# Optimization experiments

Measured on AMD Instinct MI355X. Metric: run time of the kernel, lower is better.

Reference implementation:

```python
import jax, jax.numpy as jnp
import numpy as np


def setup_inputs() -> dict:
    key = jax.random.key(0)
    ks = jax.random.split(key, 7)
    B, T, C, D = 8, 2048, 1024, 128
    x = jax.random.normal(ks[0], (B, T, C), dtype=jnp.float32)
    # torch nn.Linear weights are [out_features, in_features]
    s = 1.0 / np.sqrt(C)
    Wq = jax.random.normal(ks[1], (D, C), dtype=jnp.float32) * s
    bq = jax.random.normal(ks[2], (D,), dtype=jnp.float32) * s
    Wk = jax.random.normal(ks[3], (D, C), dtype=jnp.float32) * s
    bk = jax.random.normal(ks[4], (D,), dtype=jnp.float32) * s
    Wv = jax.random.normal(ks[5], (D, C), dtype=jnp.float32) * s
    bv = jax.random.normal(ks[6], (D,), dtype=jnp.float32) * s
    return {"x": x, "Wq": Wq, "bq": bq, "Wk": Wk, "bk": bk, "Wv": Wv, "bv": bv}


def reference(x, Wq, bq, Wk, bk, Wv, bv):
    B, T, C = x.shape
    q = jnp.einsum('btc,dc->btd', x, Wq) + bq  # [B,T,D]
    k = jnp.einsum('btc,dc->btd', x, Wk) + bk
    v = jnp.einsum('btc,dc->btd', x, Wv) + bv
    scores = jnp.einsum('btd,bsd->bts', q, k)  # [B,T,T]
    causal = jnp.tril(jnp.ones((T, T), dtype=bool))
    masked = jnp.where(causal, scores, -jnp.inf)
    # NOTE: original scales by sqrt(key.weight.shape[-1]) == sqrt(emb_dim), AFTER masking
    scale = jnp.asarray(C, dtype=x.dtype) ** 0.5
    attn = jax.nn.softmax(masked / scale, axis=-1)
    return jnp.einsum('bts,bsd->btd', attn, v)
```

## Files before the change

### kernel.cpp

```cpp
#include <hip/hip_runtime.h>
#include <hip/hip_bf16.h>
#include <math.h>

typedef __bf16 bf16_t;
typedef __bf16 bf16x4 __attribute__((ext_vector_type(4)));
typedef __bf16 bf16x8 __attribute__((ext_vector_type(8)));
typedef float  f32x4  __attribute__((ext_vector_type(4)));
typedef float  f32x16 __attribute__((ext_vector_type(16)));
typedef int    v2i    __attribute__((ext_vector_type(2)));

static constexpr int Bz = 8, Tt = 2048, Cc = 1024, Dd = 128;
static constexpr int Mm = Bz * Tt;
static constexpr int NT128 = Tt / 128;

__device__ __forceinline__ bf16x8 lds_read8(const char* base, int byte) {
    return *(const bf16x8*)(base + byte);
}

__device__ __forceinline__ bf16x8 cvt8(float4 a, float4 b) {
    bf16x8 r;
    r[0] = (bf16_t)a.x; r[1] = (bf16_t)a.y; r[2] = (bf16_t)a.z; r[3] = (bf16_t)a.w;
    r[4] = (bf16_t)b.x; r[5] = (bf16_t)b.y; r[6] = (bf16_t)b.z; r[7] = (bf16_t)b.w;
    return r;
}

__device__ __forceinline__ unsigned cvtpk(float lo, float hi) {
    unsigned r;
    asm("v_cvt_pk_bf16_f32 %0, %1, %2" : "=v"(r) : "v"(lo), "v"(hi));
    return r;
}

typedef const __attribute__((address_space(1))) unsigned int* as1_u32p;
typedef __attribute__((address_space(3))) unsigned int* as3_u32p;

__device__ __forceinline__ void gload_lds16(const bf16_t* g, bf16_t* l) {
    __builtin_amdgcn_global_load_lds((as1_u32p)(const void*)g, (as3_u32p)(void*)l, 16, 0, 0);
}

__global__ __launch_bounds__(256) void wcvt_kernel(
    const float* __restrict__ Wq, const float* __restrict__ Wk,
    const float* __restrict__ Wv, bf16_t* __restrict__ Wp)
{
    int g = (blockIdx.x * 256 + threadIdx.x) * 4;
    int n = g >> 10;
    int k = g & 1023;
    int sel = n >> 7;
    const float* W = (sel == 0) ? Wq : (sel == 1) ? Wk : Wv;
    float4 f = *(const float4*)(W + (size_t)(n & 127) * 1024 + k);
    bf16x4 o; o[0] = (bf16_t)f.x; o[1] = (bf16_t)f.y; o[2] = (bf16_t)f.z; o[3] = (bf16_t)f.w;
    int ktile = k >> 6, kk = (k >> 5) & 1, hi = (k >> 3) & 3, e = k & 7;
    int ng = n >> 4, cg = ng / 12, ngl = ng % 12, lo = n & 15;
    size_t addr = (size_t)(((((ktile * 2 + cg) * 12 + ngl) * 2 + kk) * 4 + hi) * 16 + lo) * 8 + e;
    *(bf16x4*)(Wp + addr) = o;
}

__global__ __launch_bounds__(512, 4) void qkv_fused(
    const float* __restrict__ x, const bf16_t* __restrict__ Wp,
    const float* __restrict__ bq, const float* __restrict__ bk, const float* __restrict__ bv,
    bf16_t* __restrict__ qo, bf16_t* __restrict__ ko, bf16_t* __restrict__ vTo)
{
    const int m0  = blockIdx.x * 64;
    const int cg  = blockIdx.y;
    const int tid = threadIdx.x;
    const int lane = tid & 63;
    const int wv  = tid >> 6;
    const int wr  = wv >> 2;
    const int cw  = wv & 3;
    const int lo  = lane & 15;
    const int hi  = lane >> 4;

    __shared__ bf16_t Wl[2][12 * 2 * 512];
    __shared__ bf16_t Xs[2][64 * 64];

    f32x4 zero4 = {0.f, 0.f, 0.f, 0.f};
    f32x4 acc[2][3];
    #pragma unroll
    for (int i = 0; i < 2; i++)
        #pragma unroll
        for (int j = 0; j < 3; j++) acc[i][j] = zero4;

    const int xrow = tid >> 3;
    const int xcol = (tid & 7) * 8;

    float4 fx[2];
    auto load_x = [&](int t) {
        const float4* s = (const float4*)(x + (size_t)(m0 + xrow) * Cc + t * 64 + xcol);
        fx[0] = s[0]; fx[1] = s[1];
    };
    auto write_x = [&](int buf) {
        int byte = (xrow * 128 + xcol * 2) ^ ((xrow & 7) << 4);
        *(bf16x8*)((char*)Xs[buf] + byte) = cvt8(fx[0], fx[1]);
    };
    auto stage_W = [&](int buf, int t) {
        const bf16_t* base = Wp + (size_t)(t * 2 + cg) * 12288;
        #pragma unroll
        for (int i = 0; i < 3; i++) {
            int c = i * 8 + wv;
            gload_lds16(base + c * 512 + lane * 8, Wl[buf] + c * 512);
        }
    };
    auto compute = [&](int buf) {
        #pragma unroll
        for (int kk = 0; kk < 2; kk++) {
            int r0 = wr * 32 + lo;
            int r1 = wr * 32 + 16 + lo;
            bf16x8 af0 = lds_read8((char*)Xs[buf], (r0 * 128 + kk * 64 + hi * 16) ^ ((r0 & 7) << 4));
            bf16x8 af1 = lds_read8((char*)Xs[buf], (r1 * 128 + kk * 64 + hi * 16) ^ ((r1 & 7) << 4));
            #pragma unroll
            for (int j = 0; j < 3; j++) {
                bf16x8 bf = *(const bf16x8*)(Wl[buf] + ((cw * 3 + j) * 2 + kk) * 512 + lane * 8);
                acc[0][j] = __builtin_amdgcn_mfma_f32_16x16x32_bf16(af0, bf, acc[0][j], 0, 0, 0);
                acc[1][j] = __builtin_amdgcn_mfma_f32_16x16x32_bf16(af1, bf, acc[1][j], 0, 0, 0);
            }
        }
    };

    load_x(0);
    stage_W(0, 0);
    write_x(0);
    asm volatile("s_waitcnt lgkmcnt(0)" ::: "memory");
    __builtin_amdgcn_s_barrier();

    #pragma unroll 1
    for (int t = 0; t < 16; t++) {
        const int buf = t & 1;
        if (t < 15) {
            load_x(t + 1);
            stage_W(buf ^ 1, t + 1);
            asm volatile("s_waitcnt vmcnt(5)" ::: "memory");
        } else {
            asm volatile("s_waitcnt vmcnt(0)" ::: "memory");
        }
        __builtin_amdgcn_sched_barrier(0);
        compute(buf);
        if (t < 15) {
            write_x(buf ^ 1);
            asm volatile("s_waitcnt lgkmcnt(0)" ::: "memory");
            __builtin_amdgcn_s_barrier();
        }
    }

    #pragma unroll
    for (int j = 0; j < 3; j++) {
        int n = cg * 192 + cw * 48 + j * 16 + lo;
        int tsel = n >> 7, d = n & 127;
        const float* bp = (tsel == 0) ? bq : (tsel == 1) ? bk : bv;
        float bb = bp[d];
        #pragma unroll
        for (int i = 0; i < 2; i++)
            #pragma unroll
            for (int r = 0; r < 4; r++) {
                int m = m0 + wr * 32 + i * 16 + hi * 4 + r;
                float v = acc[i][j][r] + bb;
                if (tsel == 0)      qo[(size_t)m * Dd + d] = (bf16_t)v;
                else if (tsel == 1) ko[(size_t)m * Dd + d] = (bf16_t)v;
                else                vTo[(size_t)d * Mm + m] = (bf16_t)v;
            }
    }
}

__global__ __launch_bounds__(256, 2) void attn_kernel(
    const bf16_t* __restrict__ qi, const bf16_t* __restrict__ ki,
    const bf16_t* __restrict__ vTi,
    float* __restrict__ Opart, float* __restrict__ Mpart, float* __restrict__ Lpart,
    int nsplit)
{
    const int g   = blockIdx.x;
    const int per = nsplit * 8;
    const int qt  = (NT128 - 1) - g / per;
    const int rem = g % per;
    const int s   = rem >> 3;
    const int b   = rem & 7;
    const int nt  = 2 * qt + 2;
    const int t_lo = (s * nt) / nsplit;
    const int t_hi = ((s + 1) * nt) / nsplit;

    const int q0   = qt * 128;
    const int tid  = threadIdx.x;
    const int lane = tid & 63;
    const int w    = tid >> 6;
    const int rq   = lane & 31;
    const int dh   = lane >> 5;

    float* Ob = Opart + ((size_t)s * Mm + (size_t)b * Tt + q0) * Dd;
    float* Mb = Mpart + (size_t)s * Mm + (size_t)b * Tt + q0;
    float* Lb = Lpart + (size_t)s * Mm + (size_t)b * Tt + q0;

    if (t_lo >= t_hi) {
        float4 z = {0.f, 0.f, 0.f, 0.f};
        #pragma unroll
        for (int i = 0; i < 16; i++)
            ((float4*)Ob)[i * 256 + tid] = z;
        if (tid < 128) { Mb[tid] = -INFINITY; Lb[tid] = 0.f; }
        return;
    }

    __shared__ __align__(16) char smem[65536];

    const float SCALE = 1.4426950408889634f / 32.0f;
    const int qg = q0 + w * 32 + rq;
    const int qwmax = q0 + w * 32 + 31;

    bf16x8 qf[8];
    {
        const bf16_t* qrow = qi + (size_t)(b * Tt + qg) * Dd;
        #pragma unroll
        for (int ks = 0; ks < 8; ks++)
            qf[ks] = *(const bf16x8*)(qrow + ks * 16 + dh * 8);
    }

    f32x16 accO[4];
    #pragma unroll
    for (int ds = 0; ds < 4; ds++)
        #pragma unroll
        for (int e = 0; e < 16; e++) accO[ds][e] = 0.f;
    float mrun = -INFINITY, lrun = 0.f;

    const int krow = tid >> 2;
    const int kcol = (tid & 3) * 32;
    const int vrow = tid >> 1;
    const int vcol = (tid & 1) * 32;

    bf16x8 kr[4], vr[4];
    auto load_kv = [&](int t) {
        const int kv0 = t * 64;
        const bf16_t* ksrc = ki + (size_t)(b * Tt + kv0 + krow) * Dd + kcol;
        #pragma unroll
        for (int i = 0; i < 4; i++) kr[i] = *(const bf16x8*)(ksrc + i * 8);
        const bf16_t* vsrc = vTi + (size_t)vrow * Mm + (b * Tt + kv0 + vcol);
        #pragma unroll
        for (int i = 0; i < 4; i++) vr[i] = *(const bf16x8*)(vsrc + i * 8);
    };
    auto write_kv = [&](int buf) {
        char* Ksb = smem + buf * 16384;
        char* Vsb = smem + 32768 + buf * 16384;
        #pragma unroll
        for (int i = 0; i < 4; i++) {
            int byte = (krow * 256 + (kcol + i * 8) * 2) ^ ((krow & 15) << 4);
            *(bf16x8*)(Ksb + byte) = kr[i];
        }
        const int vlr = vrow & 63;
        const int vlc = (vrow >> 6) * 64 + vcol;
        #pragma unroll
        for (int i = 0; i < 4; i++) {
            int byte = (vlr * 256 + (vlc + i * 8) * 2) ^ ((vlr & 15) << 4);
            *(bf16x8*)(Vsb + byte) = vr[i];
        }
    };

    load_kv(t_lo);
    write_kv(0);
    int buf = 0;

    for (int t = t_lo; t < t_hi; t++) {
        const int kv0 = t * 64;
        const bool more = (t + 1 < t_hi);
        __syncthreads();
        if (more) load_kv(t + 1);

        if (kv0 <= qwmax) {
            const char* Ksb = smem + buf * 16384;
            const char* Vsb = smem + 32768 + buf * 16384;

            f32x16 accS0, accS1;
            #pragma unroll
            for (int e = 0; e < 16; e++) { accS0[e] = 0.f; accS1[e] = 0.f; }
            #pragma unroll
            for (int ks = 0; ks < 8; ks++) {
                int colb = (ks * 16 + dh * 8) * 2;
                bf16x8 kf0 = lds_read8(Ksb, ((rq)      * 256 + colb) ^ ((rq & 15) << 4));
                bf16x8 kf1 = lds_read8(Ksb, ((32 + rq) * 256 + colb) ^ ((rq & 15) << 4));
                accS0 = __builtin_amdgcn_mfma_f32_32x32x16_bf16(kf0, qf[ks], accS0, 0, 0, 0);
                accS1 = __builtin_amdgcn_mfma_f32_32x32x16_bf16(kf1, qf[ks], accS1, 0, 0, 0);
            }

            float pl[32];
            #pragma unroll
            for (int e = 0; e < 16; e++) {
                pl[e]      = accS0[e] * SCALE;
                pl[16 + e] = accS1[e] * SCALE;
            }
            if (kv0 + 63 > qg) {
                #pragma unroll
                for (int e = 0; e < 16; e++) {
                    int kg = kv0 + 8 * (e >> 2) + (e & 3) + 4 * dh;
                    if (kg > qg)      pl[e]      = -INFINITY;
                    if (kg + 32 > qg) pl[16 + e] = -INFINITY;
                }
            }

            float mt = pl[0];
            #pragma unroll
            for (int e = 1; e < 32; e++) mt = fmaxf(mt, pl[e]);
            mt = fmaxf(mt, __shfl_xor(mt, 32, 64));
            float mnew = fmaxf(mrun, mt);
            float muse = (mnew == -INFINITY) ? 0.f : mnew;
            float alpha = exp2f(mrun - muse);
            mrun = mnew;
            float ps = 0.f;
            #pragma unroll
            for (int e = 0; e < 32; e++) {
                float pv = exp2f(pl[e] - muse);
                pl[e] = pv;
                ps += pv;
            }
            lrun = alpha * lrun + ps;
            #pragma unroll
            for (int ds = 0; ds < 4; ds++)
                #pragma unroll
                for (int e = 0; e < 16; e++) accO[ds][e] *= alpha;

            unsigned u0[8], u1[8];
            #pragma unroll
            for (int gg = 0; gg < 8; gg++) {
                u0[gg] = cvtpk(pl[4 * gg + 0], pl[4 * gg + 1]);
                u1[gg] = cvtpk(pl[4 * gg + 2], pl[4 * gg + 3]);
            }
            bf16x8 pa[4];
            #pragma unroll
            for (int ks = 0; ks < 4; ks++) {
                v2i rA = __builtin_amdgcn_permlane32_swap((int)u0[2 * ks], (int)u0[2 * ks + 1], false, false);
                v2i rB = __builtin_amdgcn_permlane32_swap((int)u1[2 * ks], (int)u1[2 * ks + 1], false, false);
                union { unsigned wd[4]; bf16x8 v; } pu;
                pu.wd[0] = (unsigned)rA[0];
                pu.wd[1] = (unsigned)rB[0];
                pu.wd[2] = (unsigned)rA[1];
                pu.wd[3] = (unsigned)rB[1];
                pa[ks] = pu.v;
            }

            #pragma unroll
            for (int ds = 0; ds < 4; ds++) {
                int row  = (ds & 1) * 32 + rq;
                int cb   = (ds >> 1) * 64;
                #pragma unroll
                for (int ks = 0; ks < 4; ks++) {
                    int colb = (cb + ks * 16 + dh * 8) * 2;
                    bf16x8 vf = lds_read8(Vsb, (row * 256 + colb) ^ ((row & 15) << 4));
                    accO[ds] = __builtin_amdgcn_mfma_f32_32x32x16_bf16(vf, pa[ks], accO[ds], 0, 0, 0);
                }
            }
        }

        __syncthreads();
        if (more) write_kv(buf ^ 1);
        buf ^= 1;
    }

    __syncthreads();

    lrun += __shfl_xor(lrun, 32, 64);

    char* slab = smem + w * 8192;
    #pragma unroll
    for (int half = 0; half < 2; half++) {
        #pragma unroll
        for (int dsl = 0; dsl < 2; dsl++) {
            #pragma unroll
            for (int e = 0; e < 16; e++) {
                int d = 8 * (e >> 2) + (e & 3) + 4 * dh + 32 * dsl;
                int byte = (rq * 256 + d * 4) ^ ((rq & 15) << 4);
                *(float*)(slab + byte) = accO[half * 2 + dsl][e];
            }
        }
        __builtin_amdgcn_s_waitcnt(0);
        #pragma unroll
        for (int i = 0; i < 8; i++) {
            int dd = 32 * dh + 4 * i;
            int byte = (rq * 256 + dd * 4) ^ ((rq & 15) << 4);
            float4 val = *(float4*)(slab + byte);
            *(float4*)(Ob + (size_t)(w * 32 + rq) * Dd + half * 64 + dd) = val;
        }
        __builtin_amdgcn_s_waitcnt(0);
    }

    if (lane < 32) {
        Mb[w * 32 + rq] = mrun;
        Lb[w * 32 + rq] = lrun;
    }
}

__global__ __launch_bounds__(256) void combine_kernel(
    const float* __restrict__ Opart, const float* __restrict__ Mpart,
    const float* __restrict__ Lpart, float* __restrict__ out, int nsplit)
{
    int t   = blockIdx.x * 256 + threadIdx.x;
    int row = t >> 5;
    int dq  = (t & 31) << 2;
    float M = -INFINITY;
    for (int s = 0; s < nsplit; s++)
        M = fmaxf(M, Mpart[(size_t)s * Mm + row]);
    float L = 0.f;
    float o0 = 0.f, o1 = 0.f, o2 = 0.f, o3 = 0.f;
    for (int s = 0; s < nsplit; s++) {
        float ms = Mpart[(size_t)s * Mm + row];
        float ws = (ms == -INFINITY) ? 0.f : exp2f(ms - M);
        L += ws * Lpart[(size_t)s * Mm + row];
        float4 p = *(const float4*)(Opart + ((size_t)s * Mm + row) * Dd + dq);
        o0 += ws * p.x; o1 += ws * p.y; o2 += ws * p.z; o3 += ws * p.w;
    }
    float inv = 1.0f / L;
    float4 r; r.x = o0 * inv; r.y = o1 * inv; r.z = o2 * inv; r.w = o3 * inv;
    *(float4*)(out + (size_t)row * Dd + dq) = r;
}

extern "C" void kernel_launch(void* const* d_in, const int* in_sizes, int n_in,
                              void* d_out, int out_size, void* d_ws, size_t ws_size,
                              hipStream_t stream)
{
    const float* x  = (const float*)d_in[0];
    const float* Wq = (const float*)d_in[1];
    const float* bq = (const float*)d_in[2];
    const float* Wk = (const float*)d_in[3];
    const float* bk = (const float*)d_in[4];
    const float* Wv = (const float*)d_in[5];
    const float* bv = (const float*)d_in[6];
    float* out = (float*)d_out;

    bf16_t* qb = (bf16_t*)d_ws;
    bf16_t* kb = qb + (size_t)Mm * Dd;
    bf16_t* vT = kb + (size_t)Mm * Dd;
    bf16_t* Wp = vT + (size_t)Mm * Dd;
    char* p = (char*)(Wp + (size_t)384 * Cc);

    auto need = [&](int ns) {
        return (size_t)3 * Mm * Dd * 2 + (size_t)384 * Cc * 2
             + (size_t)ns * Mm * Dd * 4 + (size_t)ns * Mm * 8;
    };
    int nsplit = 4;
    while (nsplit > 1 && need(nsplit) > ws_size) nsplit >>= 1;

    float* Opart = (float*)p;
    float* Mpart = (float*)(p + (size_t)nsplit * Mm * Dd * 4);
    float* Lpart = Mpart + (size_t)nsplit * Mm;

    wcvt_kernel<<<dim3(384), 256, 0, stream>>>(Wq, Wk, Wv, Wp);
    qkv_fused<<<dim3(256, 2), 512, 0, stream>>>(x, Wp, bq, bk, bv, qb, kb, vT);
    attn_kernel<<<dim3(NT128 * nsplit * Bz), 256, 0, stream>>>(qb, kb, vT, Opart, Mpart, Lpart, nsplit);
    combine_kernel<<<dim3(Mm * 32 / 256), 256, 0, stream>>>(Opart, Mpart, Lpart, out, nsplit);
}
```

Baseline: 69.11 us.

## Load QKV weights straight into registers, halve block to four waves

The QKV projection kernel stops staging weight tiles through LDS with global_load_lds. Each wave now loads its own weight fragments into registers, double-buffered across K-steps, and the block shrinks from 8 to 4 waves, each covering all 64 rows (acc 4x3). This removes LDS traffic and capacity used for weights and lets each wave reuse its weight fragments across more rows. In exchange it needs more VGPRs for the register-resident weights and accumulators, and each thread converts twice as much of x.

```diff
diff --git a/kernel.cpp b/kernel.cpp
--- a/kernel.cpp
+++ b/kernel.cpp
@@ -28,13 +28,6 @@
     unsigned r;
     asm("v_cvt_pk_bf16_f32 %0, %1, %2" : "=v"(r) : "v"(lo), "v"(hi));
     return r;
-}
-
-typedef const __attribute__((address_space(1))) unsigned int* as1_u32p;
-typedef __attribute__((address_space(3))) unsigned int* as3_u32p;
-
-__device__ __forceinline__ void gload_lds16(const bf16_t* g, bf16_t* l) {
-    __builtin_amdgcn_global_load_lds((as1_u32p)(const void*)g, (as3_u32p)(void*)l, 16, 0, 0);
 }
 
 __global__ __launch_bounds__(256) void wcvt_kernel(
@@ -54,7 +47,7 @@
     *(bf16x4*)(Wp + addr) = o;
 }
 
-__global__ __launch_bounds__(512, 4) void qkv_fused(
+__global__ __launch_bounds__(256, 4) void qkv_fused(
     const float* __restrict__ x, const bf16_t* __restrict__ Wp,
     const float* __restrict__ bq, const float* __restrict__ bk, const float* __restrict__ bv,
     bf16_t* __restrict__ qo, bf16_t* __restrict__ ko, bf16_t* __restrict__ vTo)
@@ -63,80 +56,89 @@
     const int cg  = blockIdx.y;
     const int tid = threadIdx.x;
     const int lane = tid & 63;
-    const int wv  = tid >> 6;
-    const int wr  = wv >> 2;
-    const int cw  = wv & 3;
+    const int cw  = tid >> 6;
     const int lo  = lane & 15;
     const int hi  = lane >> 4;
 
-    __shared__ bf16_t Wl[2][12 * 2 * 512];
     __shared__ bf16_t Xs[2][64 * 64];
 
     f32x4 zero4 = {0.f, 0.f, 0.f, 0.f};
-    f32x4 acc[2][3];
+    f32x4 acc[4][3];
     #pragma unroll
-    for (int i = 0; i < 2; i++)
+    for (int i = 0; i < 4; i++)
         #pragma unroll
         for (int j = 0; j < 3; j++) acc[i][j] = zero4;
 
-    const int xrow = tid >> 3;
-    const int xcol = (tid & 7) * 8;
-
-    float4 fx[2];
+    const int xrow  = tid >> 2;
+    const int xcolf = (tid & 3) * 16;
+    const float* xbase = x + (size_t)(m0 + xrow) * Cc + xcolf;
+
+    float4 fx0, fx1, fx2, fx3;
     auto load_x = [&](int t) {
-        const float4* s = (const float4*)(x + (size_t)(m0 + xrow) * Cc + t * 64 + xcol);
-        fx[0] = s[0]; fx[1] = s[1];
-    };
+        const float4* s = (const float4*)(xbase + t * 64);
+        fx0 = s[0]; fx1 = s[1]; fx2 = s[2]; fx3 = s[3];
+    };
+    const int xb0 = (xrow * 128 + xcolf * 2) ^ ((xrow & 7) << 4);
+    const int xb1 = (xrow * 128 + xcolf * 2 + 16) ^ ((xrow & 7) << 4);
     auto write_x = [&](int buf) {
-        int byte = (xrow * 128 + xcol * 2) ^ ((xrow & 7) << 4);
-        *(bf16x8*)((char*)Xs[buf] + byte) = cvt8(fx[0], fx[1]);
-    };
-    auto stage_W = [&](int buf, int t) {
-        const bf16_t* base = Wp + (size_t)(t * 2 + cg) * 12288;
-        #pragma unroll
-        for (int i = 0; i < 3; i++) {
-            int c = i * 8 + wv;
-            gload_lds16(base + c * 512 + lane * 8, Wl[buf] + c * 512);
-        }
-    };
-    auto compute = [&](int buf) {
+        *(bf16x8*)((char*)Xs[buf] + xb0) = cvt8(fx0, fx1);
+        *(bf16x8*)((char*)Xs[buf] + xb1) = cvt8(fx2, fx3);
+    };
+
+    bf16x8 WA[2][3], WB[2][3];
+    auto loadW = [&](bf16x8 (&dst)[2][3], int t) {
+        const bf16_t* base = Wp + (size_t)(t * 2 + cg) * 12288 + lane * 8;
+        #pragma unroll
+        for (int j = 0; j < 3; j++)
+            #pragma unroll
+            for (int kk = 0; kk < 2; kk++)
+                dst[kk][j] = *(const bf16x8*)(base + ((cw * 3 + j) * 2 + kk) * 512);
+    };
+    auto compute = [&](int buf, const bf16x8 (&Wf)[2][3]) {
         #pragma unroll
         for (int kk = 0; kk < 2; kk++) {
-            int r0 = wr * 32 + lo;
-            int r1 = wr * 32 + 16 + lo;
-            bf16x8 af0 = lds_read8((char*)Xs[buf], (r0 * 128 + kk * 64 + hi * 16) ^ ((r0 & 7) << 4));
-            bf16x8 af1 = lds_read8((char*)Xs[buf], (r1 * 128 + kk * 64 + hi * 16) ^ ((r1 & 7) << 4));
-            #pragma unroll
-            for (int j = 0; j < 3; j++) {
-                bf16x8 bf = *(const bf16x8*)(Wl[buf] + ((cw * 3 + j) * 2 + kk) * 512 + lane * 8);
-                acc[0][j] = __builtin_amdgcn_mfma_f32_16x16x32_bf16(af0, bf, acc[0][j], 0, 0, 0);
-                acc[1][j] = __builtin_amdgcn_mfma_f32_16x16x32_bf16(af1, bf, acc[1][j], 0, 0, 0);
-            }
+            bf16x8 af[4];
+            #pragma unroll
+            for (int i = 0; i < 4; i++) {
+                int r = i * 16 + lo;
+                af[i] = lds_read8((char*)Xs[buf], (r * 128 + kk * 64 + hi * 16) ^ ((r & 7) << 4));
+            }
+            #pragma unroll
+            for (int i = 0; i < 4; i++)
+                #pragma unroll
+                for (int j = 0; j < 3; j++)
+                    acc[i][j] = __builtin_amdgcn_mfma_f32_16x16x32_bf16(af[i], Wf[kk][j], acc[i][j], 0, 0, 0);
         }
     };
 
     load_x(0);
-    stage_W(0, 0);
+    loadW(WA, 0);
     write_x(0);
+    loadW(WB, 1);
     asm volatile("s_waitcnt lgkmcnt(0)" ::: "memory");
     __builtin_amdgcn_s_barrier();
 
     #pragma unroll 1
-    for (int t = 0; t < 16; t++) {
-        const int buf = t & 1;
-        if (t < 15) {
+    for (int tp = 0; tp < 8; tp++) {
+        {
+            const int t = 2 * tp;
             load_x(t + 1);
-            stage_W(buf ^ 1, t + 1);
-            asm volatile("s_waitcnt vmcnt(5)" ::: "memory");
-        } else {
-            asm volatile("s_waitcnt vmcnt(0)" ::: "memory");
-        }
-        __builtin_amdgcn_sched_barrier(0);
-        compute(buf);
-        if (t < 15) {
-            write_x(buf ^ 1);
+            compute(0, WA);
+            if (t + 2 < 16) loadW(WA, t + 2);
+            write_x(1);
             asm volatile("s_waitcnt lgkmcnt(0)" ::: "memory");
             __builtin_amdgcn_s_barrier();
+        }
+        {
+            const int t = 2 * tp + 1;
+            if (t + 1 < 16) load_x(t + 1);
+            compute(1, WB);
+            if (t + 2 < 16) loadW(WB, t + 2);
+            if (t + 1 < 16) {
+                write_x(0);
+                asm volatile("s_waitcnt lgkmcnt(0)" ::: "memory");
+                __builtin_amdgcn_s_barrier();
+            }
         }
     }
 
@@ -147,10 +149,10 @@
         const float* bp = (tsel == 0) ? bq : (tsel == 1) ? bk : bv;
         float bb = bp[d];
         #pragma unroll
-        for (int i = 0; i < 2; i++)
+        for (int i = 0; i < 4; i++)
             #pragma unroll
             for (int r = 0; r < 4; r++) {
-                int m = m0 + wr * 32 + i * 16 + hi * 4 + r;
+                int m = m0 + i * 16 + hi * 4 + r;
                 float v = acc[i][j][r] + bb;
                 if (tsel == 0)      qo[(size_t)m * Dd + d] = (bf16_t)v;
                 else if (tsel == 1) ko[(size_t)m * Dd + d] = (bf16_t)v;
@@ -435,7 +437,7 @@
     float* Lpart = Mpart + (size_t)nsplit * Mm;
 
     wcvt_kernel<<<dim3(384), 256, 0, stream>>>(Wq, Wk, Wv, Wp);
-    qkv_fused<<<dim3(256, 2), 512, 0, stream>>>(x, Wp, bq, bk, bv, qb, kb, vT);
+    qkv_fused<<<dim3(256, 2), 256, 0, stream>>>(x, Wp, bq, bk, bv, qb, kb, vT);
     attn_kernel<<<dim3(NT128 * nsplit * Bz), 256, 0, stream>>>(qb, kb, vT, Opart, Mpart, Lpart, nsplit);
     combine_kernel<<<dim3(Mm * 32 / 256), 256, 0, stream>>>(Opart, Mpart, Lpart, out, nsplit);
 }
```

Measured after the change: 91.12 us. +31.9%, slower.
